# Performance work log

Measured on AMD Instinct MI355X. Metric: run time of the kernel, lower is better.

## Reference

```python
import jax, jax.numpy as jnp
import numpy as np

NUM_FREQS = 10
NUM_VOXELS = 512
N_POINTS = 262144
IN_DIM = 3
INPUT_CH = IN_DIM + 2 * NUM_FREQS * IN_DIM  # 63


def posenc(x, num_freqs):
    # NeRF positional encoding: [x, sin(x*2^0), cos(x*2^0), ..., sin(x*2^(F-1)), cos(x*2^(F-1))]
    freqs = (2.0 ** jnp.arange(num_freqs)).astype(x.dtype)           # (F,)
    xf = x[:, None, :] * freqs[None, :, None]                        # (N, F, D)
    sc = jnp.stack([jnp.sin(xf), jnp.cos(xf)], axis=2)               # (N, F, 2, D)
    return jnp.concatenate([x, sc.reshape(x.shape[0], -1)], axis=-1)  # (N, D + 2*F*D)


def setup_inputs() -> dict:
    key = jax.random.key(0)
    k_x, k_w, k_v = jax.random.split(key, 3)
    X = jax.random.normal(k_x, (N_POINTS, IN_DIM), dtype=jnp.float32)
    # linear_mappings reshaped to (3*num_voxels, input_ch), used as Linear weight (no bias)
    W = jax.random.normal(k_w, (3 * NUM_VOXELS, INPUT_CH), dtype=jnp.float32) * 0.02
    row_ids = jnp.arange(N_POINTS, dtype=jnp.int64 if jax.config.jax_enable_x64 else jnp.int32)
    voxel_ids = jax.random.randint(k_v, (N_POINTS,), 0, NUM_VOXELS)
    return {"X": X, "W": W, "row_ids": row_ids, "voxel_ids": voxel_ids}


def reference(X, W, row_ids, voxel_ids):
    encoded_X = posenc(X, NUM_FREQS)                      # (N, 63)
    rgb_clusters = encoded_X @ W.T                        # (N, 3*num_voxels) -- wasteful dense GEMM
    # col_indices per selected row: [3v, 3v+1, 3v+2]
    cols = jnp.stack([3 * voxel_ids, 3 * voxel_ids + 1, 3 * voxel_ids + 2], axis=1)  # (M, 3)
    vals = rgb_clusters[row_ids[:, None], cols]           # (M, 3)
    rgb = jnp.zeros((X.shape[0], 3), dtype=X.dtype)
    rgb = rgb.at[row_ids].set(vals)
    return rgb
```

## Files before the change

### kernel.cpp

```cpp
#include <hip/hip_runtime.h>
#include <math.h>

#define N_POINTS   262144
#define NUM_FREQS  10
#define NUM_VOXELS 512


typedef _Float16 half2v __attribute__((ext_vector_type(2)));

__device__ __forceinline__ half2v u2h(unsigned int u) {
    union { unsigned int u; half2v h; } c; c.u = u; return c.h;
}

__device__ __forceinline__ float dot2acc(half2v a, half2v b, float acc) {
#if __has_builtin(__builtin_amdgcn_fdot2)
    return __builtin_amdgcn_fdot2(a, b, acc, false);
#else
    return acc + (float)a[0] * (float)b[0] + (float)a[1] * (float)b[1];
#endif
}

__global__ __launch_bounds__(1024) void pack_w(
    const float* __restrict__ W, _Float16* __restrict__ Wp)
{
    const int gid = blockIdx.x * 1024 + threadIdx.x;
    const int v = gid / 192, e = gid % 192;
    const int row = e >> 6, col = e & 63;
    Wp[v * 192 + e] = (col < 63) ? (_Float16)W[v * 189 + row * 63 + col]
                                 : (_Float16)0.0f;
}

__device__ __forceinline__ void posenc_pack_dot(
    float x0, float x1, float x2, const _Float16* __restrict__ Wp, int v,
    float& a0, float& a1, float& a2)
{
    half2v eh[32];
#define SETE(p, val) eh[(p) >> 1][(p) & 1] = (_Float16)(val)
    SETE(0, x0); SETE(1, x1); SETE(2, x2);
    SETE(63, 0.0f);

    float s0, c0, s1, c1, s2, c2;
    __sincosf(x0, &s0, &c0);
    __sincosf(x1, &s1, &c1);
    __sincosf(x2, &s2, &c2);
    #pragma unroll
    for (int f = 0; f < NUM_FREQS; ++f) {
        const int b = 3 + 6*f;
        SETE(b+0, s0); SETE(b+1, s1); SETE(b+2, s2);
        SETE(b+3, c0); SETE(b+4, c1); SETE(b+5, c2);
        if (f < NUM_FREQS - 1) {
            const float ns0 = 2.0f*s0*c0, nc0 = c0*c0 - s0*s0;
            const float ns1 = 2.0f*s1*c1, nc1 = c1*c1 - s1*s1;
            const float ns2 = 2.0f*s2*c2, nc2 = c2*c2 - s2*s2;
            s0 = ns0; c0 = nc0; s1 = ns1; c1 = nc1; s2 = ns2; c2 = nc2;
        }
    }
#undef SETE

    const uint4* __restrict__ wb = (const uint4*)(Wp + (size_t)v * 192);
    float acc[3];
    #pragma unroll
    for (int r = 0; r < 3; ++r) {
        float a = 0.0f;
        #pragma unroll
        for (int k = 0; k < 8; ++k) {
            const uint4 q = wb[r * 8 + k];
            a = dot2acc(u2h(q.x), eh[4*k + 0], a);
            a = dot2acc(u2h(q.y), eh[4*k + 1], a);
            a = dot2acc(u2h(q.z), eh[4*k + 2], a);
            a = dot2acc(u2h(q.w), eh[4*k + 3], a);
        }
        acc[r] = a;
    }
    a0 = acc[0]; a1 = acc[1]; a2 = acc[2];
}

__global__ __launch_bounds__(1024) void voxlin_fused(
    const float* __restrict__ X,
    const _Float16* __restrict__ Wp,
    const int* __restrict__ row_ids,
    const int* __restrict__ voxel_ids,
    float* __restrict__ out)
{
    __shared__ float4 pts[1024];
    __shared__ int    hist[NUM_VOXELS];
    __shared__ int    cur[NUM_VOXELS];
    __shared__ int    wsum[8];

    const int t    = threadIdx.x;
    const int lane = t & 63;
    const int wid  = t >> 6;
    const int i    = blockIdx.x * 1024 + t;

    const int   v  = voxel_ids[i];
    const float x0 = X[3*i + 0];
    const float x1 = X[3*i + 1];
    const float x2 = X[3*i + 2];
    const int   r  = row_ids[i];

    if (t < NUM_VOXELS) hist[t] = 0;
    __syncthreads();
    atomicAdd(&hist[v], 1);
    __syncthreads();

    int c = 0, incl = 0;
    if (t < NUM_VOXELS) {
        c = hist[t];
        incl = c;
        #pragma unroll
        for (int d = 1; d < 64; d <<= 1) {
            int n = __shfl_up(incl, d);
            if (lane >= d) incl += n;
        }
        if (lane == 63) wsum[wid] = incl;
    }
    __syncthreads();
    if (t < 64) {
        int s = (lane < 8) ? wsum[lane] : 0;
        #pragma unroll
        for (int d = 1; d < 8; d <<= 1) {
            int n = __shfl_up(s, d);
            if (lane >= d) s += n;
        }
        int excl = __shfl_up(s, 1);
        if (lane == 0) excl = 0;
        if (lane < 8) wsum[lane] = excl;
    }
    __syncthreads();
    if (t < NUM_VOXELS) cur[t] = wsum[wid] + incl - c;
    __syncthreads();

    const int mypos = atomicAdd(&cur[v], 1);
    pts[mypos] = make_float4(x0, x1, x2, __int_as_float(v));
    __syncthreads();

    const float4 q  = pts[t];
    const int    sv = __float_as_int(q.w);
    float a0, a1, a2;
    posenc_pack_dot(q.x, q.y, q.z, Wp, sv, a0, a1, a2);

    pts[t] = make_float4(a0, a1, a2, 0.0f);
    __syncthreads();

    const float4 res = pts[mypos];
    out[3*r + 0] = res.x;
    out[3*r + 1] = res.y;
    out[3*r + 2] = res.z;
}

__global__ __launch_bounds__(256) void voxlin_fallback(
    const float* __restrict__ X, const float* __restrict__ W,
    const int* __restrict__ row_ids, const int* __restrict__ voxel_ids,
    float* __restrict__ out)
{
    const int i = blockIdx.x * 256 + threadIdx.x;
    if (i >= N_POINTS) return;
    const float x0 = X[3*i], x1 = X[3*i+1], x2 = X[3*i+2];
    const int v = voxel_ids[i];
    const float* __restrict__ w0 = W + v * 189;
    const float* __restrict__ w1 = w0 + 63;
    const float* __restrict__ w2 = w0 + 126;
    float a0 = x0*w0[0] + x1*w0[1] + x2*w0[2];
    float a1 = x0*w1[0] + x1*w1[1] + x2*w1[2];
    float a2 = x0*w2[0] + x1*w2[1] + x2*w2[2];
    float s0, c0, s1, c1, s2, c2;
    __sincosf(x0, &s0, &c0); __sincosf(x1, &s1, &c1); __sincosf(x2, &s2, &c2);
    #pragma unroll
    for (int f = 0; f < NUM_FREQS; ++f) {
        const int b = 3 + 6*f;
        a0 += s0*w0[b] + s1*w0[b+1] + s2*w0[b+2] + c0*w0[b+3] + c1*w0[b+4] + c2*w0[b+5];
        a1 += s0*w1[b] + s1*w1[b+1] + s2*w1[b+2] + c0*w1[b+3] + c1*w1[b+4] + c2*w1[b+5];
        a2 += s0*w2[b] + s1*w2[b+1] + s2*w2[b+2] + c0*w2[b+3] + c1*w2[b+4] + c2*w2[b+5];
        if (f < NUM_FREQS - 1) {
            const float ns0 = 2.0f*s0*c0, nc0 = c0*c0 - s0*s0;
            const float ns1 = 2.0f*s1*c1, nc1 = c1*c1 - s1*s1;
            const float ns2 = 2.0f*s2*c2, nc2 = c2*c2 - s2*s2;
            s0 = ns0; c0 = nc0; s1 = ns1; c1 = nc1; s2 = ns2; c2 = nc2;
        }
    }
    const int rr = row_ids[i];
    out[3*rr] = a0; out[3*rr+1] = a1; out[3*rr+2] = a2;
}

extern "C" void kernel_launch(void* const* d_in, const int* in_sizes, int n_in,
                              void* d_out, int out_size, void* d_ws, size_t ws_size,
                              hipStream_t stream) {
    const float* X         = (const float*)d_in[0];
    const float* W         = (const float*)d_in[1];
    const int*   row_ids   = (const int*)d_in[2];
    const int*   voxel_ids = (const int*)d_in[3];
    float*       out       = (float*)d_out;

    const size_t need = (size_t)NUM_VOXELS * 192 * sizeof(_Float16);

    if (ws_size >= need) {
        _Float16* Wp = (_Float16*)d_ws;
        pack_w<<<96, 1024, 0, stream>>>(W, Wp);
        voxlin_fused<<<N_POINTS / 1024, 1024, 0, stream>>>(X, Wp, row_ids, voxel_ids, out);
    } else {
        voxlin_fallback<<<(N_POINTS + 255) / 256, 256, 0, stream>>>(X, W, row_ids, voxel_ids, out);
    }
}
```

Measured before the change: 71.62 us.

## Fold weight packing into main kernel via cooperative launch and grid sync

```diff
diff --git a/kernel.cpp b/kernel.cpp
--- a/kernel.cpp
+++ b/kernel.cpp
@@ -1,4 +1,5 @@
 #include <hip/hip_runtime.h>
+#include <hip/hip_cooperative_groups.h>
 #include <math.h>
 
 #define N_POINTS   262144
@@ -18,16 +19,6 @@
 #else
     return acc + (float)a[0] * (float)b[0] + (float)a[1] * (float)b[1];
 #endif
-}
-
-__global__ __launch_bounds__(1024) void pack_w(
-    const float* __restrict__ W, _Float16* __restrict__ Wp)
-{
-    const int gid = blockIdx.x * 1024 + threadIdx.x;
-    const int v = gid / 192, e = gid % 192;
-    const int row = e >> 6, col = e & 63;
-    Wp[v * 192 + e] = (col < 63) ? (_Float16)W[v * 189 + row * 63 + col]
-                                 : (_Float16)0.0f;
 }
 
 __device__ __forceinline__ void posenc_pack_dot(
@@ -75,12 +66,14 @@
     a0 = acc[0]; a1 = acc[1]; a2 = acc[2];
 }
 
-__global__ __launch_bounds__(1024) void voxlin_fused(
+template <bool COOP>
+__global__ __launch_bounds__(1024) void voxlin_k(
     const float* __restrict__ X,
-    const _Float16* __restrict__ Wp,
+    _Float16* __restrict__ Wp,
     const int* __restrict__ row_ids,
     const int* __restrict__ voxel_ids,
-    float* __restrict__ out)
+    float* __restrict__ out,
+    const float* __restrict__ W)
 {
     __shared__ float4 pts[1024];
     __shared__ int    hist[NUM_VOXELS];
@@ -91,6 +84,16 @@
     const int lane = t & 63;
     const int wid  = t >> 6;
     const int i    = blockIdx.x * 1024 + t;
+
+    if (COOP) {
+        if (t < 384) {
+            const int gid = blockIdx.x * 384 + t;
+            const int v = gid / 192, e = gid % 192;
+            const int row = e >> 6, col = e & 63;
+            Wp[v * 192 + e] = (col < 63) ? (_Float16)W[v * 189 + row * 63 + col]
+                                         : (_Float16)0.0f;
+        }
+    }
 
     const int   v  = voxel_ids[i];
     const float x0 = X[3*i + 0];
@@ -134,6 +137,11 @@
     pts[mypos] = make_float4(x0, x1, x2, __int_as_float(v));
     __syncthreads();
 
+    if (COOP) {
+        __threadfence();
+        cooperative_groups::this_grid().sync();
+    }
+
     const float4 q  = pts[t];
     const int    sv = __float_as_int(q.w);
     float a0, a1, a2;
@@ -146,6 +154,16 @@
     out[3*r + 0] = res.x;
     out[3*r + 1] = res.y;
     out[3*r + 2] = res.z;
+}
+
+__global__ __launch_bounds__(1024) void pack_w(
+    const float* __restrict__ W, _Float16* __restrict__ Wp)
+{
+    const int gid = blockIdx.x * 1024 + threadIdx.x;
+    const int v = gid / 192, e = gid % 192;
+    const int row = e >> 6, col = e & 63;
+    Wp[v * 192 + e] = (col < 63) ? (_Float16)W[v * 189 + row * 63 + col]
+                                 : (_Float16)0.0f;
 }
 
 __global__ __launch_bounds__(256) void voxlin_fallback(
@@ -195,8 +213,16 @@
 
     if (ws_size >= need) {
         _Float16* Wp = (_Float16*)d_ws;
-        pack_w<<<96, 1024, 0, stream>>>(W, Wp);
-        voxlin_fused<<<N_POINTS / 1024, 1024, 0, stream>>>(X, Wp, row_ids, voxel_ids, out);
+        void* args[] = { (void*)&X, (void*)&Wp, (void*)&row_ids,
+                         (void*)&voxel_ids, (void*)&out, (void*)&W };
+        hipError_t err = hipLaunchCooperativeKernel(
+            (void*)voxlin_k<true>, dim3(N_POINTS / 1024), dim3(1024),
+            args, 0, stream);
+        if (err != hipSuccess) {
+            pack_w<<<96, 1024, 0, stream>>>(W, Wp);
+            voxlin_k<false><<<N_POINTS / 1024, 1024, 0, stream>>>(
+                X, Wp, row_ids, voxel_ids, out, W);
+        }
     } else {
         voxlin_fallback<<<(N_POINTS + 255) / 256, 256, 0, stream>>>(X, W, row_ids, voxel_ids, out);
     }
```

Result: slower. 162.4 us (+126.7%).
